# Optimization experiments

Hardware: AMD Instinct MI355X
Metric: run time of the kernel (lower is better)

## Reference

```python
import jax, jax.numpy as jnp
import numpy as np

B, NQ, NK, D_IN, HD = 1, 16384, 7933, 1024, 512
R = 0.3  # keep-top-r fraction used for the quantile threshold


def _l2norm(x):
    # matches F.normalize(p=2, dim=-1, eps=1e-12)
    n = jnp.linalg.norm(x, axis=-1, keepdims=True)
    return x / jnp.maximum(n, 1e-12)


def setup_inputs() -> dict:
    key = jax.random.key(0)
    ks = jax.random.split(key, 10)
    s = 0.02
    return {
        "query": jax.random.normal(ks[0], (B, NQ, D_IN), jnp.float32),
        "key_x": jax.random.normal(ks[1], (B, NK, D_IN), jnp.float32),
        "wq_w": jax.random.normal(ks[2], (HD, D_IN), jnp.float32) * s,
        "wq_b": jnp.zeros((HD,), jnp.float32),
        "wk_w": jax.random.normal(ks[3], (HD, D_IN), jnp.float32) * s,
        "wk_b": jnp.zeros((HD,), jnp.float32),
        "wa_w": jax.random.normal(ks[4], (1, NK), jnp.float32) * s,
        "wa_b": jnp.zeros((1,), jnp.float32),
        "cls_w": jax.random.normal(ks[5], (1, HD), jnp.float32) * s,
        "cls_b": jnp.zeros((1,), jnp.float32),
    }


def reference(query, key_x, wq_w, wq_b, wk_w, wk_b, wa_w, wa_b, cls_w, cls_b):
    # WQ / WK: Linear + Tanh
    q = jnp.tanh(jnp.einsum("bnd,hd->bnh", query, wq_w) + wq_b)   # [B,NQ,HD]
    k = jnp.tanh(jnp.einsum("bnd,hd->bnh", key_x, wk_w) + wk_b)   # [B,NK,HD]
    # normalized dot-product scores
    A = jnp.einsum("bqh,bkh->bqk", _l2norm(q), _l2norm(k))        # [B,NQ,NK]
    # WA: Linear(NK -> 1)
    A1 = jnp.einsum("bqk,ok->bqo", A, wa_w) + wa_b                # [B,NQ,1]
    # quantile threshold from batch 0 (torch: sorted ascending, index -int(r*NQ))
    thre = jax.lax.stop_gradient(jnp.sort(A1[0, :, 0])[-int(R * NQ)])
    A1 = jnp.where(A1 > thre, A1, 0.0)                            # F.threshold(., thre, 0)
    attn = jax.nn.softmax(A1, axis=1)                             # softmax over NQ (zeros included)
    attn_t = jnp.transpose(attn, (0, 2, 1))                       # [B,1,NQ]
    z = jnp.matmul(attn_t, q).reshape(-1, HD)                     # [B,HD]
    y_prob = z @ cls_w.T + cls_b                                  # [B,1]
    return (y_prob, attn_t)
```

## Files before the change

kernel.cpp:

```cpp
#include <hip/hip_runtime.h>
#include <math.h>

#define NQ 16384
#define NK 7933
#define DI 1024
#define HD 512
#define RANK_TARGET 11469

typedef __bf16 bf16x8 __attribute__((ext_vector_type(8)));
typedef float  f32x4  __attribute__((ext_vector_type(4)));

#define GLOAD_LDS16(g, l)                                                     \
  __builtin_amdgcn_global_load_lds(                                           \
      (const __attribute__((address_space(1))) void*)(g),                     \
      (__attribute__((address_space(3))) void*)(l), 16, 0, 0)

__device__ __forceinline__ unsigned mapf(float f) {
  unsigned b = __float_as_uint(f);
  return (b & 0x80000000u) ? ~b : (b | 0x80000000u);
}

__global__ void conv_w(const float* __restrict__ wq, const float* __restrict__ wk,
                       __bf16* __restrict__ wqbf, __bf16* __restrict__ wkbf,
                       unsigned* __restrict__ zero_region) {
  if (blockIdx.x == 0) {
    for (int j = threadIdx.x; j < 1088; j += 256) zero_region[j] = 0u;
  }
  const int W8 = HD * DI / 8;
  int i = blockIdx.x * 256 + threadIdx.x;
  const float* s; __bf16* d; int j;
  if (i < W8) { s = wq; d = wqbf; j = i; }
  else        { s = wk; d = wkbf; j = i - W8; }
  float4 a = ((const float4*)s)[2 * j];
  float4 b = ((const float4*)s)[2 * j + 1];
  bf16x8 o;
  o[0] = (__bf16)a.x; o[1] = (__bf16)a.y; o[2] = (__bf16)a.z; o[3] = (__bf16)a.w;
  o[4] = (__bf16)b.x; o[5] = (__bf16)b.y; o[6] = (__bf16)b.z; o[7] = (__bf16)b.w;
  ((bf16x8*)d)[j] = o;
}

template <bool FUSE_A1>
__global__ __launch_bounds__(512, 4)
void gemm_f32a_tanh(const float* __restrict__ A, const __bf16* __restrict__ B,
                    const float* __restrict__ bias, float* __restrict__ C, int M,
                    const float* __restrict__ v, float* __restrict__ A1dot,
                    float* __restrict__ A1ss) {
  constexpr int K = DI;
  constexpr int N = HD;
  __shared__ __align__(16) __bf16 sA[64 * 64];
  __shared__ __align__(16) __bf16 sB[256 * 64];

  const int tid  = threadIdx.x;
  const int lane = tid & 63;
  const int wave = tid >> 6;
  const int wr = wave >> 2;
  const int wc = wave & 3;
  const int m0 = blockIdx.x * 64, n0 = blockIdx.y * 256;

  const int arow = tid >> 3;
  const int acb  = tid & 7;
  __bf16* aw = &sA[arow * 64 + ((acb ^ (arow & 7)) << 3)];
  int ga = m0 + arow; if (ga > M - 1) ga = M - 1;
  const float* ap = A + (size_t)ga * K + acb * 8;

  const int srow = lane >> 3;
  const int scol = ((lane & 7) ^ srow) << 3;

  const int lrow = lane & 15;
  const int chi  = lane >> 4;

  f32x4 acc[2][4] = {};

  for (int kk = 0; kk < K; kk += 64) {
    float4 x0 = *(const float4*)(ap + kk);
    float4 x1 = *(const float4*)(ap + kk + 4);
    __syncthreads();
    bf16x8 o;
    o[0] = (__bf16)x0.x; o[1] = (__bf16)x0.y; o[2] = (__bf16)x0.z; o[3] = (__bf16)x0.w;
    o[4] = (__bf16)x1.x; o[5] = (__bf16)x1.y; o[6] = (__bf16)x1.z; o[7] = (__bf16)x1.w;
    *(bf16x8*)aw = o;
#pragma unroll
    for (int c = 0; c < 4; ++c) {
      int seg = wave * 4 + c;
      GLOAD_LDS16(B + (size_t)(n0 + seg * 8 + srow) * K + kk + scol, &sB[seg * 512]);
    }
    __syncthreads();
#pragma unroll
    for (int ks = 0; ks < 64; ks += 32) {
      const int cc = (ks >> 3) + chi;
      const int sw = ((cc ^ (lrow & 7)) << 3);
      bf16x8 af[2], bfr[4];
#pragma unroll
      for (int mi = 0; mi < 2; ++mi)
        af[mi] = *(const bf16x8*)(&sA[(wr * 32 + mi * 16 + lrow) * 64 + sw]);
#pragma unroll
      for (int ni = 0; ni < 4; ++ni)
        bfr[ni] = *(const bf16x8*)(&sB[(wc * 64 + ni * 16 + lrow) * 64 + sw]);
#pragma unroll
      for (int mi = 0; mi < 2; ++mi)
#pragma unroll
        for (int ni = 0; ni < 4; ++ni)
          acc[mi][ni] = __builtin_amdgcn_mfma_f32_16x16x32_bf16(af[mi], bfr[ni], acc[mi][ni], 0, 0, 0);
    }
  }

  const int rbase = m0 + wr * 32 + ((lane >> 4) << 2);
  const int cbase = n0 + wc * 64 + (lane & 15);
  float b4[4], v4[4];
#pragma unroll
  for (int ni = 0; ni < 4; ++ni) {
    b4[ni] = bias[cbase + ni * 16];
    if constexpr (FUSE_A1) v4[ni] = v[cbase + ni * 16];
  }
#pragma unroll
  for (int mi = 0; mi < 2; ++mi) {
#pragma unroll
    for (int r = 0; r < 4; ++r) {
      int grow = rbase + mi * 16 + r;
      if (grow < M) {
        float pd = 0.f, pss = 0.f;
#pragma unroll
        for (int ni = 0; ni < 4; ++ni) {
          float val = tanhf(acc[mi][ni][r] + b4[ni]);
          C[(size_t)grow * N + cbase + ni * 16] = val;
          if constexpr (FUSE_A1) { pd += val * v4[ni]; pss += val * val; }
        }
        if constexpr (FUSE_A1) {
#pragma unroll
          for (int off = 1; off < 16; off <<= 1) {
            pd += __shfl_xor(pd, off);
            pss += __shfl_xor(pss, off);
          }
          if ((lane & 15) == 0) {
            atomicAdd(&A1dot[grow], pd);
            atomicAdd(&A1ss[grow], pss);
          }
        }
      }
    }
  }
}

__global__ __launch_bounds__(256)
void reduce_v_zero(const float* __restrict__ kt, const float* __restrict__ wa,
                   float* __restrict__ v, int M, uint2* __restrict__ zr) {
  {
    int g = blockIdx.x * 256 + threadIdx.x;
    uint2 zz; zz.x = 0u; zz.y = 0u;
    zr[g] = zz;
    if (g < 24576 - 16384) zr[16384 + g] = zz;
  }
  __shared__ float vpart[4][512];
  const int tid = threadIdx.x, lane = tid & 63, wave = tid >> 6;
  const int gw = blockIdx.x * 4 + wave;
  const int tw = gridDim.x * 4;
  float acc[8] = {0, 0, 0, 0, 0, 0, 0, 0};
  for (int r = gw; r < M; r += tw) {
    const float4* p = (const float4*)(kt + (size_t)r * HD + lane * 8);
    float4 x = p[0], y = p[1];
    float ss = x.x * x.x + x.y * x.y + x.z * x.z + x.w * x.w
             + y.x * y.x + y.y * y.y + y.z * y.z + y.w * y.w;
#pragma unroll
    for (int off = 32; off; off >>= 1) ss += __shfl_xor(ss, off);
    float s = wa[r] / fmaxf(sqrtf(ss), 1e-12f);
    acc[0] += s * x.x; acc[1] += s * x.y; acc[2] += s * x.z; acc[3] += s * x.w;
    acc[4] += s * y.x; acc[5] += s * y.y; acc[6] += s * y.z; acc[7] += s * y.w;
  }
#pragma unroll
  for (int j = 0; j < 8; ++j) vpart[wave][lane * 8 + j] = acc[j];
  __syncthreads();
  for (int c = tid; c < 512; c += 256)
    atomicAdd(&v[c], vpart[0][c] + vpart[1][c] + vpart[2][c] + vpart[3][c]);
}

__global__ __launch_bounds__(1024)
void select_kernel(const float* __restrict__ A1dot, const float* __restrict__ A1ss,
                   const float* __restrict__ wa_b, float* __restrict__ A1,
                   unsigned* __restrict__ keyg, float* __restrict__ scf) {
  __shared__ unsigned wred1[16], wred2[16], wred3[16];
  __shared__ unsigned s_res;
  const int t = threadIdx.x, lane = t & 63, wave = t >> 6;
  const float wab = wa_b[0];
  unsigned kloc[16];
#pragma unroll 4
  for (int j = 0; j < 16; ++j) {
    int i = j * 1024 + t;
    float d = A1dot[i], ss = A1ss[i];
    float a1 = d / fmaxf(sqrtf(ss), 1e-12f) + wab;
    A1[i] = a1;
    unsigned k = mapf(a1);
    kloc[j] = k;
    keyg[i] = k;
  }
  if (t == 0) s_res = 0u;
  __syncthreads();

  for (int b = 30; b >= 0; b -= 2) {
    const unsigned res = s_res;
    const unsigned t1 = res | (1u << b);
    const unsigned t2 = res | (2u << b);
    const unsigned t3 = res | (3u << b);
    unsigned c1 = 0, c2 = 0, c3 = 0;
#pragma unroll
    for (int j = 0; j < 16; ++j) {
      unsigned k = kloc[j];
      c1 += (k < t1); c2 += (k < t2); c3 += (k < t3);
    }
#pragma unroll
    for (int off = 32; off; off >>= 1) {
      c1 += __shfl_xor(c1, off);
      c2 += __shfl_xor(c2, off);
      c3 += __shfl_xor(c3, off);
    }
    if (lane == 0) { wred1[wave] = c1; wred2[wave] = c2; wred3[wave] = c3; }
    __syncthreads();
    if (t == 0) {
      unsigned C1 = 0, C2 = 0, C3 = 0;
      for (int w = 0; w < 16; ++w) { C1 += wred1[w]; C2 += wred2[w]; C3 += wred3[w]; }
      unsigned nr = res;
      if (C3 <= RANK_TARGET)      nr = t3;
      else if (C2 <= RANK_TARGET) nr = t2;
      else if (C1 <= RANK_TARGET) nr = t1;
      s_res = nr;
    }
    __syncthreads();
  }
  if (t == 0) {
    unsigned key = s_res;
    unsigned bits = (key & 0x80000000u) ? (key ^ 0x80000000u) : ~key;
    scf[0] = __uint_as_float(bits);
  }
}

__global__ __launch_bounds__(256)
void expz(const float* __restrict__ A1, const float* __restrict__ qt,
          float* __restrict__ scf, float* __restrict__ e_out,
          float* __restrict__ z) {
  __shared__ float vpart[4][512];
  __shared__ float esum[4];
  const int tid = threadIdx.x, lane = tid & 63, wave = tid >> 6;
  const float thre = scf[0];
  const int gw = blockIdx.x * 4 + wave;
  const int tw = gridDim.x * 4;
  float acc[8] = {0, 0, 0, 0, 0, 0, 0, 0};
  float es = 0.f;
  for (int r = gw; r < NQ; r += tw) {
    float x = A1[r]; x = (x > thre) ? x : 0.f;
    float e = expf(x - thre);
    if (lane == 0) e_out[r] = e;
    es += e;
    const float4* p = (const float4*)(qt + (size_t)r * HD + lane * 8);
    float4 u = p[0], w = p[1];
    acc[0] += e * u.x; acc[1] += e * u.y; acc[2] += e * u.z; acc[3] += e * u.w;
    acc[4] += e * w.x; acc[5] += e * w.y; acc[6] += e * w.z; acc[7] += e * w.w;
  }
  if (lane == 0) esum[wave] = es;
#pragma unroll
  for (int j = 0; j < 8; ++j) vpart[wave][lane * 8 + j] = acc[j];
  __syncthreads();
  for (int c = tid; c < 512; c += 256)
    atomicAdd(&z[c], vpart[0][c] + vpart[1][c] + vpart[2][c] + vpart[3][c]);
  if (tid == 0) atomicAdd(&scf[2], esum[0] + esum[1] + esum[2] + esum[3]);
}

__global__ __launch_bounds__(256)
void finalize(float* __restrict__ attn, const float* __restrict__ scf,
              const float* __restrict__ z, const float* __restrict__ cls_w,
              const float* __restrict__ cls_b, float* __restrict__ y) {
  const float invZ = 1.f / scf[2];
  if (blockIdx.x < 64) {
    int i = blockIdx.x * 256 + threadIdx.x;
    attn[i] *= invZ;
  } else if (threadIdx.x < 64) {
    const int lane = threadIdx.x;
    const float4* zp = (const float4*)(z + lane * 8);
    const float4* wp = (const float4*)(cls_w + lane * 8);
    float4 a = zp[0], b = zp[1], c = wp[0], d = wp[1];
    float dot = a.x * c.x + a.y * c.y + a.z * c.z + a.w * c.w
              + b.x * d.x + b.y * d.y + b.z * d.z + b.w * d.w;
#pragma unroll
    for (int off = 32; off; off >>= 1) dot += __shfl_xor(dot, off);
    if (lane == 0) y[0] = dot * invZ + cls_b[0];
  }
}

#define OFF_WQBF 0u
#define OFF_WKBF 1048576u
#define OFF_A1D  1048576u
#define OFF_A1S  1114112u
#define OFF_KEY  1179648u
#define OFF_A1   35651584u
#define OFF_V    35717120u
#define OFF_Z    35719168u
#define OFF_SC   35721216u
#define OFF_KT   51968256u
#define OFF_QT   35721472u

extern "C" void kernel_launch(void* const* d_in, const int* in_sizes, int n_in,
                              void* d_out, int out_size, void* d_ws, size_t ws_size,
                              hipStream_t stream) {
  const float* query = (const float*)d_in[0];
  const float* key_x = (const float*)d_in[1];
  const float* wq_w  = (const float*)d_in[2];
  const float* wq_b  = (const float*)d_in[3];
  const float* wk_w  = (const float*)d_in[4];
  const float* wk_b  = (const float*)d_in[5];
  const float* wa_w  = (const float*)d_in[6];
  const float* wa_b  = (const float*)d_in[7];
  const float* cls_w = (const float*)d_in[8];
  const float* cls_b = (const float*)d_in[9];
  float* out = (float*)d_out;

  char* ws = (char*)d_ws;
  __bf16* wqbf  = (__bf16*)(ws + OFF_WQBF);
  __bf16* wkbf  = (__bf16*)(ws + OFF_WKBF);
  float*  A1dot = (float*)(ws + OFF_A1D);
  float*  A1ss  = (float*)(ws + OFF_A1S);
  unsigned* keyg = (unsigned*)(ws + OFF_KEY);
  float*  A1    = (float*)(ws + OFF_A1);
  float*  v     = (float*)(ws + OFF_V);
  float*  z     = (float*)(ws + OFF_Z);
  float*  scf   = (float*)(ws + OFF_SC);
  float*  ktanh = (float*)(ws + OFF_KT);
  float*  qtanh = (float*)(ws + OFF_QT);
  float*  out_attn = out + 1;

  conv_w<<<512, 256, 0, stream>>>(wq_w, wk_w, wqbf, wkbf, (unsigned*)v);

  gemm_f32a_tanh<false><<<dim3(124, 2), 512, 0, stream>>>(
      key_x, wkbf, wk_b, ktanh, NK, nullptr, nullptr, nullptr);

  reduce_v_zero<<<64, 256, 0, stream>>>(ktanh, wa_w, v, NK, (uint2*)A1dot);

  gemm_f32a_tanh<true><<<dim3(256, 2), 512, 0, stream>>>(
      query, wqbf, wq_b, qtanh, NQ, v, A1dot, A1ss);

  select_kernel<<<1, 1024, 0, stream>>>(A1dot, A1ss, wa_b, A1, keyg, scf);

  expz<<<256, 256, 0, stream>>>(A1, qtanh, scf, out_attn, z);

  finalize<<<65, 256, 0, stream>>>(out_attn, scf, z, cls_w, cls_b, out);
}
```

Before: 254.2 us.

## Double-buffer weight tiles in LDS and load A fragments directly to registers

The projection GEMM now double-buffers the bf16 weight tile in shared memory, issuing the next k-step's async global-to-LDS loads before computing the current one, so there is one barrier per iteration instead of two. The f32 activation operand is no longer staged through LDS. Each wave loads its own MFMA A-fragment rows directly from global memory and converts them to bf16 in registers. This removes the LDS round trip and one sync for A, but the per-lane global loads are narrower and strided, and different column-waves reload the same rows. Shared memory use for B doubles, which may affect occupancy.

```diff
diff --git a/kernel.cpp b/kernel.cpp
--- a/kernel.cpp
+++ b/kernel.cpp
@@ -18,6 +18,13 @@
 __device__ __forceinline__ unsigned mapf(float f) {
   unsigned b = __float_as_uint(f);
   return (b & 0x80000000u) ? ~b : (b | 0x80000000u);
+}
+
+__device__ __forceinline__ bf16x8 cvt8(float4 a, float4 b) {
+  bf16x8 o;
+  o[0] = (__bf16)a.x; o[1] = (__bf16)a.y; o[2] = (__bf16)a.z; o[3] = (__bf16)a.w;
+  o[4] = (__bf16)b.x; o[5] = (__bf16)b.y; o[6] = (__bf16)b.z; o[7] = (__bf16)b.w;
+  return o;
 }
 
 __global__ void conv_w(const float* __restrict__ wq, const float* __restrict__ wk,
@@ -47,8 +54,7 @@
                     float* __restrict__ A1ss) {
   constexpr int K = DI;
   constexpr int N = HD;
-  __shared__ __align__(16) __bf16 sA[64 * 64];
-  __shared__ __align__(16) __bf16 sB[256 * 64];
+  __shared__ __align__(16) __bf16 sB[2][256 * 64];
 
   const int tid  = threadIdx.x;
   const int lane = tid & 63;
@@ -57,50 +63,83 @@
   const int wc = wave & 3;
   const int m0 = blockIdx.x * 64, n0 = blockIdx.y * 256;
 
-  const int arow = tid >> 3;
-  const int acb  = tid & 7;
-  __bf16* aw = &sA[arow * 64 + ((acb ^ (arow & 7)) << 3)];
-  int ga = m0 + arow; if (ga > M - 1) ga = M - 1;
-  const float* ap = A + (size_t)ga * K + acb * 8;
-
   const int srow = lane >> 3;
   const int scol = ((lane & 7) ^ srow) << 3;
 
   const int lrow = lane & 15;
   const int chi  = lane >> 4;
 
+  const float* arow0;
+  const float* arow1;
+  {
+    int r0 = m0 + wr * 32 + lrow;       if (r0 > M - 1) r0 = M - 1;
+    int r1 = m0 + wr * 32 + 16 + lrow;  if (r1 > M - 1) r1 = M - 1;
+    arow0 = A + (size_t)r0 * K + chi * 8;
+    arow1 = A + (size_t)r1 * K + chi * 8;
+  }
+
   f32x4 acc[2][4] = {};
 
-  for (int kk = 0; kk < K; kk += 64) {
-    float4 x0 = *(const float4*)(ap + kk);
-    float4 x1 = *(const float4*)(ap + kk + 4);
-    __syncthreads();
-    bf16x8 o;
-    o[0] = (__bf16)x0.x; o[1] = (__bf16)x0.y; o[2] = (__bf16)x0.z; o[3] = (__bf16)x0.w;
-    o[4] = (__bf16)x1.x; o[5] = (__bf16)x1.y; o[6] = (__bf16)x1.z; o[7] = (__bf16)x1.w;
-    *(bf16x8*)aw = o;
-#pragma unroll
-    for (int c = 0; c < 4; ++c) {
-      int seg = wave * 4 + c;
-      GLOAD_LDS16(B + (size_t)(n0 + seg * 8 + srow) * K + kk + scol, &sB[seg * 512]);
-    }
-    __syncthreads();
-#pragma unroll
-    for (int ks = 0; ks < 64; ks += 32) {
-      const int cc = (ks >> 3) + chi;
+#pragma unroll
+  for (int c = 0; c < 4; ++c) {
+    int seg = wave * 4 + c;
+    GLOAD_LDS16(B + (size_t)(n0 + seg * 8 + srow) * K + scol, &sB[0][seg * 512]);
+  }
+  __syncthreads();
+
+  int buf = 0;
+  for (int t = 0; t < 16; ++t) {
+    const int kk = t * 64;
+    if (t < 15) {
+#pragma unroll
+      for (int c = 0; c < 4; ++c) {
+        int seg = wave * 4 + c;
+        GLOAD_LDS16(B + (size_t)(n0 + seg * 8 + srow) * K + kk + 64 + scol,
+                    &sB[buf ^ 1][seg * 512]);
+      }
+    }
+    float4 a00 = *(const float4*)(arow0 + kk);
+    float4 a01 = *(const float4*)(arow0 + kk + 4);
+    float4 a10 = *(const float4*)(arow1 + kk);
+    float4 a11 = *(const float4*)(arow1 + kk + 4);
+    float4 b00 = *(const float4*)(arow0 + kk + 32);
+    float4 b01 = *(const float4*)(arow0 + kk + 36);
+    float4 b10 = *(const float4*)(arow1 + kk + 32);
+    float4 b11 = *(const float4*)(arow1 + kk + 36);
+
+    const __bf16* sBc = sB[buf];
+    {
+      const int sw = ((chi ^ (lrow & 7)) << 3);
+      bf16x8 af0 = cvt8(a00, a01);
+      bf16x8 af1 = cvt8(a10, a11);
+      bf16x8 bfr[4];
+#pragma unroll
+      for (int ni = 0; ni < 4; ++ni)
+        bfr[ni] = *(const bf16x8*)(&sBc[(wc * 64 + ni * 16 + lrow) * 64 + sw]);
+#pragma unroll
+      for (int ni = 0; ni < 4; ++ni) {
+        acc[0][ni] = __builtin_amdgcn_mfma_f32_16x16x32_bf16(af0, bfr[ni], acc[0][ni], 0, 0, 0);
+        acc[1][ni] = __builtin_amdgcn_mfma_f32_16x16x32_bf16(af1, bfr[ni], acc[1][ni], 0, 0, 0);
+      }
+    }
+    {
+      const int cc = 4 + chi;
       const int sw = ((cc ^ (lrow & 7)) << 3);
-      bf16x8 af[2], bfr[4];
-#pragma unroll
-      for (int mi = 0; mi < 2; ++mi)
-        af[mi] = *(const bf16x8*)(&sA[(wr * 32 + mi * 16 + lrow) * 64 + sw]);
+      bf16x8 af0 = cvt8(b00, b01);
+      bf16x8 af1 = cvt8(b10, b11);
+      bf16x8 bfr[4];
 #pragma unroll
       for (int ni = 0; ni < 4; ++ni)
-        bfr[ni] = *(const bf16x8*)(&sB[(wc * 64 + ni * 16 + lrow) * 64 + sw]);
-#pragma unroll
-      for (int mi = 0; mi < 2; ++mi)
-#pragma unroll
-        for (int ni = 0; ni < 4; ++ni)
-          acc[mi][ni] = __builtin_amdgcn_mfma_f32_16x16x32_bf16(af[mi], bfr[ni], acc[mi][ni], 0, 0, 0);
+        bfr[ni] = *(const bf16x8*)(&sBc[(wc * 64 + ni * 16 + lrow) * 64 + sw]);
+#pragma unroll
+      for (int ni = 0; ni < 4; ++ni) {
+        acc[0][ni] = __builtin_amdgcn_mfma_f32_16x16x32_bf16(af0, bfr[ni], acc[0][ni], 0, 0, 0);
+        acc[1][ni] = __builtin_amdgcn_mfma_f32_16x16x32_bf16(af1, bfr[ni], acc[1][ni], 0, 0, 0);
+      }
+    }
+    if (t < 15) {
+      __syncthreads();
+      buf ^= 1;
     }
   }
 
```

After: 322.2 us. 26.7% more time.
